# Kernel tuning notes

Hardware: AMD Instinct MI355X
Metric: run time of the kernel (lower is better)

The kernel has to match this reference:

```python
import jax, jax.numpy as jnp
import numpy as np

N = 50000      # nodes
E = 800000     # random edges (self-loops appended -> E + N total)
IN = 128       # in_channels
H = 1          # heads
C = 128        # out_channels per head
NEG_SLOPE = 0.2


def setup_inputs() -> dict:
    key = jax.random.key(0)
    k1, k2, k3, k4, k5 = jax.random.split(key, 5)
    x = jax.random.normal(k1, (N, IN), jnp.float32)
    src = jax.random.randint(k2, (E,), 0, N)
    dst = jax.random.randint(k3, (E,), 0, N)
    loops = jnp.arange(N)
    # PyG 1.3.2 GATConv adds self-loops before propagate
    edge_index = jnp.stack([jnp.concatenate([src, loops]),
                            jnp.concatenate([dst, loops])]).astype(jnp.int64)
    W = jax.random.normal(k4, (IN, H * C), jnp.float32) * np.float32(1.0 / np.sqrt(IN))
    att = jax.random.normal(k5, (H, 2 * C), jnp.float32) * np.float32(0.1)
    bias = jnp.zeros((H * C,), jnp.float32)
    return {"x": x, "edge_index": edge_index, "W": W, "att": att, "bias": bias}


def reference(x, edge_index, W, att, bias):
    h = (x @ W).reshape(-1, H, C)            # [N,H,C] transformed features
    src, dst = edge_index[0], edge_index[1]  # j -> i
    hi = h[dst]                              # [Etot,H,C] x_i gather
    hj = h[src]                              # [Etot,H,C] x_j gather
    # alpha = sum(cat(x_i,x_j) * att, -1)
    alpha = (jnp.einsum('ehc,hc->eh', hi, att[:, :C])
             + jnp.einsum('ehc,hc->eh', hj, att[:, C:]))
    alpha = jax.nn.leaky_relu(alpha, NEG_SLOPE)
    # segment softmax over destination node (stable)
    m = jax.ops.segment_max(alpha, dst, num_segments=N)
    m = jnp.where(jnp.isfinite(m), m, 0.0)   # guard empty segments
    a = jnp.exp(alpha - m[dst])
    s = jax.ops.segment_sum(a, dst, num_segments=N)
    a = a / (s[dst] + 1e-16)
    # weighted scatter-add aggregation
    out = jax.ops.segment_sum(hj * a[:, :, None], dst, num_segments=N)  # [N,H,C]
    return out.reshape(-1, H * C) + bias
```

## Files before the change

kernel.cpp:

```cpp
#include <hip/hip_runtime.h>
#include <math.h>


constexpr int CH = 128;
constexpr int BNODES = 64;
constexpr int CAP = 2048;
constexpr int SCAP = 3072;
constexpr int NBMAX = 1024;
constexpr int SCHUNK = 4096;
constexpr int WTS = 136;
constexpr unsigned SENT = 0xFFFFFFFFu;

typedef __attribute__((ext_vector_type(8))) short bf16x8;
typedef __attribute__((ext_vector_type(4))) float f32x4;

static __device__ __forceinline__ unsigned short f2bf(float f) {
    unsigned u = __float_as_uint(f);
    unsigned r = (u + 0x7fffu + ((u >> 16) & 1u)) >> 16;
    return (unsigned short)r;
}

__global__ __launch_bounds__(256) void wtzero_kernel(const float* __restrict__ W,
                                                     unsigned short* __restrict__ WT,
                                                     int* __restrict__ gcur, int nb) {
    const int T = blockIdx.x * 256 + threadIdx.x;
    if (T < nb) gcur[T] = 0;
    const int k = T >> 4;
    const int n8 = (T & 15) * 8;
    const float4 a = *(const float4*)&W[k * CH + n8];
    const float4 b = *(const float4*)&W[k * CH + n8 + 4];
    WT[(n8 + 0) * WTS + k] = f2bf(a.x);
    WT[(n8 + 1) * WTS + k] = f2bf(a.y);
    WT[(n8 + 2) * WTS + k] = f2bf(a.z);
    WT[(n8 + 3) * WTS + k] = f2bf(a.w);
    WT[(n8 + 4) * WTS + k] = f2bf(b.x);
    WT[(n8 + 5) * WTS + k] = f2bf(b.y);
    WT[(n8 + 6) * WTS + k] = f2bf(b.z);
    WT[(n8 + 7) * WTS + k] = f2bf(b.w);
}

__global__ __launch_bounds__(256) void gemm_scatter_kernel(const float* __restrict__ x,
                                                           const unsigned short* __restrict__ WT,
                                                           const float* __restrict__ att,
                                                           unsigned short* __restrict__ hb,
                                                           float* __restrict__ ad,
                                                           float* __restrict__ as_,
                                                           const int* __restrict__ src,
                                                           const int* __restrict__ dst,
                                                           int* __restrict__ gcur,
                                                           unsigned* __restrict__ recs,
                                                           int n, int etot, int nb, int sb) {
    __shared__ alignas(16) unsigned char smem[52224];
    const int tid = threadIdx.x;

    if ((int)blockIdx.x >= sb) {
        unsigned short* Wl = (unsigned short*)smem;
        unsigned short* Xs = (unsigned short*)(smem + 34816);
        {
            const uint4* s = (const uint4*)WT;
            uint4* d = (uint4*)Wl;
            for (int i = tid; i < CH * WTS / 8; i += 256) d[i] = s[i];
        }

        const int lane = tid & 63, wave = tid >> 6;
        const int m = lane & 15, quad = lane >> 4;
        const int tbase = ((int)blockIdx.x - sb) * 128;
        const int srow = tid >> 2, sseg = tid & 3;

        #pragma unroll 1
        for (int half = 0; half < 2; ++half) {
            __syncthreads();
            {
                const int grow = min(tbase + half * 64 + srow, n - 1);
                const float* gx = x + (size_t)grow * CH;
                unsigned short* xd = &Xs[srow * WTS];
                #pragma unroll
                for (int i = 0; i < 8; ++i) {
                    const int c = sseg * 4 + i * 16;
                    const float4 u = *(const float4*)&gx[c];
                    ushort4 hs;
                    hs.x = f2bf(u.x); hs.y = f2bf(u.y); hs.z = f2bf(u.z); hs.w = f2bf(u.w);
                    *(ushort4*)&xd[c] = hs;
                }
            }
            __syncthreads();

            const int row0 = tbase + half * 64 + wave * 16;
            f32x4 acc[8] = {};
            #pragma unroll
            for (int t = 0; t < 4; ++t) {
                const int kb = t * 32 + quad * 8;
                const bf16x8 afr = *(const bf16x8*)&Xs[(wave * 16 + m) * WTS + kb];
                #pragma unroll
                for (int nt = 0; nt < 8; ++nt) {
                    const bf16x8 bfr = *(const bf16x8*)&Wl[(nt * 16 + m) * WTS + kb];
                    acc[nt] = __builtin_amdgcn_mfma_f32_16x16x32_bf16(afr, bfr, acc[nt], 0, 0, 0);
                }
            }

            const int rbase = row0 + quad * 4;
            float pd[4] = {}, ps[4] = {};
            #pragma unroll
            for (int nt = 0; nt < 8; ++nt) {
                const int col = nt * 16 + m;
                const float atd = att[col], ats = att[CH + col];
                #pragma unroll
                for (int r = 0; r < 4; ++r) {
                    pd[r] = fmaf(acc[nt][r], atd, pd[r]);
                    ps[r] = fmaf(acc[nt][r], ats, ps[r]);
                    const int rr = rbase + r;
                    if (rr < n) hb[(size_t)rr * CH + col] = f2bf(acc[nt][r]);
                }
            }
            #pragma unroll
            for (int r = 0; r < 4; ++r) {
                #pragma unroll
                for (int off = 8; off >= 1; off >>= 1) {
                    pd[r] += __shfl_xor(pd[r], off, 64);
                    ps[r] += __shfl_xor(ps[r], off, 64);
                }
                const int rr = rbase + r;
                if (m == 0 && rr < n) { ad[rr] = pd[r]; as_[rr] = ps[r]; }
            }
        }
    } else {
        int* hist = (int*)smem;
        int* cur = hist + NBMAX;
        unsigned* rbuf = (unsigned*)(cur + NBMAX);
        const int e0 = (int)blockIdx.x * SCHUNK;
        for (int t = tid; t < nb; t += 256) hist[t] = 0;
        __syncthreads();
        for (int i = tid; i < SCHUNK; i += 256) {
            const int e = e0 + i;
            if (e < etot) {
                const int d = dst[e];
                rbuf[i] = ((unsigned)d << 16) | (unsigned)src[e];
                atomicAdd(&hist[d >> 6], 1);
            }
        }
        __syncthreads();
        for (int t = tid; t < nb; t += 256) {
            const int h = hist[t];
            cur[t] = h ? atomicAdd(&gcur[t], h) : 0;
        }
        __syncthreads();
        for (int i = tid; i < SCHUNK; i += 256) {
            const int e = e0 + i;
            if (e < etot) {
                const unsigned r = rbuf[i];
                const int d = (int)(r >> 16);
                const int b = d >> 6;
                const int pos = atomicAdd(&cur[b], 1);
                if (pos < CAP)
                    recs[(size_t)b * CAP + pos] = ((unsigned)(d & 63) << 16) | (r & 0xffffu);
            }
        }
    }
}

__global__ __launch_bounds__(512) void aggregate_kernel(const unsigned char* __restrict__ hwb,
                                                        const float* __restrict__ ad,
                                                        const float* __restrict__ as_,
                                                        const int* __restrict__ gcur,
                                                        const unsigned* __restrict__ recs,
                                                        const float* __restrict__ bias,
                                                        float* __restrict__ out, int n) {
    __shared__ alignas(16) unsigned sorted[SCAP];
    __shared__ alignas(16) float alphas[SCAP];
    __shared__ float adl[BNODES];
    __shared__ int cnt[BNODES], ofs[BNODES], cur[BNODES];
    __shared__ int nEp_s;
    const int b = blockIdx.x;
    const int tid = threadIdx.x, lane = tid & 63, wid = tid >> 6;
    const unsigned* br = recs + (size_t)b * CAP;
    int nE = gcur[b]; if (nE > CAP) nE = CAP;
    unsigned* stash = (unsigned*)alphas;

    if (tid < BNODES) {
        cnt[tid] = 0;
        const int node = b * BNODES + tid;
        adl[tid] = (node < n) ? ad[node] : 0.f;
    }
    __syncthreads();
    for (int i = tid; i < nE; i += 512) {
        const unsigned r = br[i];
        stash[i] = r;
        atomicAdd(&cnt[r >> 16], 1);
    }
    __syncthreads();
    if (wid == 0) {
        const int c = cnt[lane];
        const int cr = (c + 15) & ~15;
        int v = cr;
        #pragma unroll
        for (int off = 1; off < 64; off <<= 1) {
            const int u = __shfl_up(v, (unsigned)off, 64);
            if (lane >= off) v += u;
        }
        ofs[lane] = v - cr;
        cur[lane] = v - cr;
        if (lane == 63) nEp_s = v;
    }
    __syncthreads();
    const int nEp = nEp_s;
    for (int i = tid; i < nEp; i += 512) sorted[i] = SENT;
    __syncthreads();
    for (int i = tid; i < nE; i += 512) {
        const unsigned r = stash[i];
        const int pos = atomicAdd(&cur[r >> 16], 1);
        sorted[pos] = r;
    }
    __syncthreads();
    for (int i = tid; i < nEp; i += 512) {
        const unsigned r = sorted[i];
        float p = 0.f;
        unsigned so = 0u;
        if (r != SENT) {
            float a = adl[r >> 16] + as_[r & 0xffffu];
            a = (a >= 0.f) ? a : 0.2f * a;
            p = __expf(a);
            so = (r & 0xffffu) << 8;
        }
        alphas[i] = p;
        sorted[i] = so;
    }
    __syncthreads();

    const unsigned lane4 = (unsigned)lane * 4u;
    for (int ln = wid; ln < BNODES; ln += 8) {
        const int node = b * BNODES + ln;
        if (node >= n) break;
        const int start = ofs[ln];
        const int endp = start + ((cnt[ln] + 15) & ~15);

        float ssum = 0.f, acc0 = 0.f, acc1 = 0.f;
        for (int e = start; e < endp; e += 16) {
            const uint4 s0 = *(const uint4*)&sorted[e];
            const uint4 s1 = *(const uint4*)&sorted[e + 4];
            const uint4 s2 = *(const uint4*)&sorted[e + 8];
            const uint4 s3 = *(const uint4*)&sorted[e + 12];
            const float4 p0 = *(const float4*)&alphas[e];
            const float4 p1 = *(const float4*)&alphas[e + 4];
            const float4 p2 = *(const float4*)&alphas[e + 8];
            const float4 p3 = *(const float4*)&alphas[e + 12];
            unsigned g[16];
            g[0]  = *(const unsigned*)(hwb + (s0.x + lane4));
            g[1]  = *(const unsigned*)(hwb + (s0.y + lane4));
            g[2]  = *(const unsigned*)(hwb + (s0.z + lane4));
            g[3]  = *(const unsigned*)(hwb + (s0.w + lane4));
            g[4]  = *(const unsigned*)(hwb + (s1.x + lane4));
            g[5]  = *(const unsigned*)(hwb + (s1.y + lane4));
            g[6]  = *(const unsigned*)(hwb + (s1.z + lane4));
            g[7]  = *(const unsigned*)(hwb + (s1.w + lane4));
            g[8]  = *(const unsigned*)(hwb + (s2.x + lane4));
            g[9]  = *(const unsigned*)(hwb + (s2.y + lane4));
            g[10] = *(const unsigned*)(hwb + (s2.z + lane4));
            g[11] = *(const unsigned*)(hwb + (s2.w + lane4));
            g[12] = *(const unsigned*)(hwb + (s3.x + lane4));
            g[13] = *(const unsigned*)(hwb + (s3.y + lane4));
            g[14] = *(const unsigned*)(hwb + (s3.z + lane4));
            g[15] = *(const unsigned*)(hwb + (s3.w + lane4));
            ssum += (p0.x + p0.y + p0.z + p0.w) + (p1.x + p1.y + p1.z + p1.w)
                  + (p2.x + p2.y + p2.z + p2.w) + (p3.x + p3.y + p3.z + p3.w);
            const float p[16] = {p0.x, p0.y, p0.z, p0.w, p1.x, p1.y, p1.z, p1.w,
                                 p2.x, p2.y, p2.z, p2.w, p3.x, p3.y, p3.z, p3.w};
            #pragma unroll
            for (int j = 0; j < 16; ++j) {
                acc0 = fmaf(p[j], __uint_as_float((g[j] & 0xffffu) << 16), acc0);
                acc1 = fmaf(p[j], __uint_as_float(g[j] & 0xffff0000u), acc1);
            }
        }
        const float inv = 1.f / (ssum + 1e-16f);
        const float2 bv = *(const float2*)&bias[lane * 2];
        float2 o;
        o.x = fmaf(acc0, inv, bv.x);
        o.y = fmaf(acc1, inv, bv.y);
        *(float2*)&out[node * CH + lane * 2] = o;
    }
}

extern "C" void kernel_launch(void* const* d_in, const int* in_sizes, int n_in,
                              void* d_out, int out_size, void* d_ws, size_t ws_size,
                              hipStream_t stream) {
    const float* x    = (const float*)d_in[0];
    const int*   ei   = (const int*)d_in[1];
    const float* W    = (const float*)d_in[2];
    const float* att  = (const float*)d_in[3];
    const float* bias = (const float*)d_in[4];
    float* out = (float*)d_out;

    const int N_   = in_sizes[0] / CH;
    const int Etot = in_sizes[1] / 2;
    const int* src = ei;
    const int* dst = ei + Etot;
    const int nb = (N_ + BNODES - 1) / BNODES;
    const int gb = (N_ + 127) / 128;
    const int sb = (Etot + SCHUNK - 1) / SCHUNK;

    char* ws = (char*)d_ws;
    size_t off = 0;
    auto alloc = [&](size_t bytes) -> void* {
        void* p = ws + off;
        off = (off + bytes + 255) & ~(size_t)255;
        return p;
    };
    unsigned short* hb = (unsigned short*)alloc((size_t)N_ * CH * sizeof(unsigned short));
    unsigned short* WT = (unsigned short*)alloc((size_t)CH * WTS * sizeof(unsigned short));
    float* ad      = (float*)alloc((size_t)N_ * sizeof(float));
    float* as_     = (float*)alloc((size_t)N_ * sizeof(float));
    int*   gcur    = (int*)  alloc((size_t)nb * sizeof(int));
    unsigned* recs = (unsigned*)alloc((size_t)nb * CAP * sizeof(unsigned));
    (void)ws_size; (void)n_in; (void)out_size;

    wtzero_kernel<<<8, 256, 0, stream>>>(W, WT, gcur, nb);
    gemm_scatter_kernel<<<sb + gb, 256, 0, stream>>>(x, WT, att, hb, ad, as_,
                                                     src, dst, gcur, recs, N_, Etot, nb, sb);
    aggregate_kernel<<<nb, 512, 0, stream>>>((const unsigned char*)hb, ad, as_, gcur, recs, bias, out, N_);
}
```

Before: 134.8 us.

## Split wavefront into half-waves gathering 8-byte rows, pad segments to 8

The aggregation loop now splits each 64-lane wavefront into two halves. Each half handles alternate edges, and every lane loads 8 bytes (four bf16 channels) instead of 4, so there are half as many gather instructions per edge pair. The partial sums are combined with a cross-half shuffle, and the lower 32 lanes write float4 outputs. Per-node segments are padded to 8 instead of 16, which wastes fewer gather slots on sentinel edges. The softmax denominator now comes from shared-memory atomics during the alpha pass, which adds LDS atomic contention in exchange for dropping the per-iteration sum.

```diff
diff --git a/kernel.cpp b/kernel.cpp
--- a/kernel.cpp
+++ b/kernel.cpp
@@ -168,6 +168,7 @@
     __shared__ alignas(16) unsigned sorted[SCAP];
     __shared__ alignas(16) float alphas[SCAP];
     __shared__ float adl[BNODES];
+    __shared__ float ssumL[BNODES];
     __shared__ int cnt[BNODES], ofs[BNODES], cur[BNODES];
     __shared__ int nEp_s;
     const int b = blockIdx.x;
@@ -178,6 +179,7 @@
 
     if (tid < BNODES) {
         cnt[tid] = 0;
+        ssumL[tid] = 0.f;
         const int node = b * BNODES + tid;
         adl[tid] = (node < n) ? ad[node] : 0.f;
     }
@@ -190,7 +192,7 @@
     __syncthreads();
     if (wid == 0) {
         const int c = cnt[lane];
-        const int cr = (c + 15) & ~15;
+        const int cr = (c + 7) & ~7;
         int v = cr;
         #pragma unroll
         for (int off = 1; off < 64; off <<= 1) {
@@ -220,21 +222,25 @@
             a = (a >= 0.f) ? a : 0.2f * a;
             p = __expf(a);
             so = (r & 0xffffu) << 8;
+            atomicAdd(&ssumL[r >> 16], p);
         }
         alphas[i] = p;
         sorted[i] = so;
     }
     __syncthreads();
 
-    const unsigned lane4 = (unsigned)lane * 4u;
+    const unsigned half = (unsigned)(lane >> 5);
+    const unsigned lo8 = (unsigned)(lane & 31) * 8u;
     for (int ln = wid; ln < BNODES; ln += 8) {
         const int node = b * BNODES + ln;
         if (node >= n) break;
         const int start = ofs[ln];
-        const int endp = start + ((cnt[ln] + 15) & ~15);
-
-        float ssum = 0.f, acc0 = 0.f, acc1 = 0.f;
-        for (int e = start; e < endp; e += 16) {
+        const int cnt8 = (cnt[ln] + 7) & ~7;
+        const int end16 = start + (cnt8 & ~15);
+
+        float a0 = 0.f, a1 = 0.f, a2 = 0.f, a3 = 0.f;
+        int e = start;
+        for (; e < end16; e += 16) {
             const uint4 s0 = *(const uint4*)&sorted[e];
             const uint4 s1 = *(const uint4*)&sorted[e + 4];
             const uint4 s2 = *(const uint4*)&sorted[e + 8];
@@ -243,39 +249,111 @@
             const float4 p1 = *(const float4*)&alphas[e + 4];
             const float4 p2 = *(const float4*)&alphas[e + 8];
             const float4 p3 = *(const float4*)&alphas[e + 12];
-            unsigned g[16];
-            g[0]  = *(const unsigned*)(hwb + (s0.x + lane4));
-            g[1]  = *(const unsigned*)(hwb + (s0.y + lane4));
-            g[2]  = *(const unsigned*)(hwb + (s0.z + lane4));
-            g[3]  = *(const unsigned*)(hwb + (s0.w + lane4));
-            g[4]  = *(const unsigned*)(hwb + (s1.x + lane4));
-            g[5]  = *(const unsigned*)(hwb + (s1.y + lane4));
-            g[6]  = *(const unsigned*)(hwb + (s1.z + lane4));
-            g[7]  = *(const unsigned*)(hwb + (s1.w + lane4));
-            g[8]  = *(const unsigned*)(hwb + (s2.x + lane4));
-            g[9]  = *(const unsigned*)(hwb + (s2.y + lane4));
-            g[10] = *(const unsigned*)(hwb + (s2.z + lane4));
-            g[11] = *(const unsigned*)(hwb + (s2.w + lane4));
-            g[12] = *(const unsigned*)(hwb + (s3.x + lane4));
-            g[13] = *(const unsigned*)(hwb + (s3.y + lane4));
-            g[14] = *(const unsigned*)(hwb + (s3.z + lane4));
-            g[15] = *(const unsigned*)(hwb + (s3.w + lane4));
-            ssum += (p0.x + p0.y + p0.z + p0.w) + (p1.x + p1.y + p1.z + p1.w)
-                  + (p2.x + p2.y + p2.z + p2.w) + (p3.x + p3.y + p3.z + p3.w);
-            const float p[16] = {p0.x, p0.y, p0.z, p0.w, p1.x, p1.y, p1.z, p1.w,
-                                 p2.x, p2.y, p2.z, p2.w, p3.x, p3.y, p3.z, p3.w};
-            #pragma unroll
-            for (int j = 0; j < 16; ++j) {
-                acc0 = fmaf(p[j], __uint_as_float((g[j] & 0xffffu) << 16), acc0);
-                acc1 = fmaf(p[j], __uint_as_float(g[j] & 0xffff0000u), acc1);
-            }
-        }
-        const float inv = 1.f / (ssum + 1e-16f);
-        const float2 bv = *(const float2*)&bias[lane * 2];
-        float2 o;
-        o.x = fmaf(acc0, inv, bv.x);
-        o.y = fmaf(acc1, inv, bv.y);
-        *(float2*)&out[node * CH + lane * 2] = o;
+            const unsigned A0 = half ? s0.y : s0.x;
+            const unsigned A1 = half ? s0.w : s0.z;
+            const unsigned A2 = half ? s1.y : s1.x;
+            const unsigned A3 = half ? s1.w : s1.z;
+            const unsigned A4 = half ? s2.y : s2.x;
+            const unsigned A5 = half ? s2.w : s2.z;
+            const unsigned A6 = half ? s3.y : s3.x;
+            const unsigned A7 = half ? s3.w : s3.z;
+            const float q0 = half ? p0.y : p0.x;
+            const float q1 = half ? p0.w : p0.z;
+            const float q2 = half ? p1.y : p1.x;
+            const float q3 = half ? p1.w : p1.z;
+            const float q4 = half ? p2.y : p2.x;
+            const float q5 = half ? p2.w : p2.z;
+            const float q6 = half ? p3.y : p3.x;
+            const float q7 = half ? p3.w : p3.z;
+            const uint2 g0 = *(const uint2*)(hwb + A0 + lo8);
+            const uint2 g1 = *(const uint2*)(hwb + A1 + lo8);
+            const uint2 g2 = *(const uint2*)(hwb + A2 + lo8);
+            const uint2 g3 = *(const uint2*)(hwb + A3 + lo8);
+            const uint2 g4 = *(const uint2*)(hwb + A4 + lo8);
+            const uint2 g5 = *(const uint2*)(hwb + A5 + lo8);
+            const uint2 g6 = *(const uint2*)(hwb + A6 + lo8);
+            const uint2 g7 = *(const uint2*)(hwb + A7 + lo8);
+            a0 = fmaf(q0, __uint_as_float(g0.x << 16), a0);
+            a1 = fmaf(q0, __uint_as_float(g0.x & 0xffff0000u), a1);
+            a2 = fmaf(q0, __uint_as_float(g0.y << 16), a2);
+            a3 = fmaf(q0, __uint_as_float(g0.y & 0xffff0000u), a3);
+            a0 = fmaf(q1, __uint_as_float(g1.x << 16), a0);
+            a1 = fmaf(q1, __uint_as_float(g1.x & 0xffff0000u), a1);
+            a2 = fmaf(q1, __uint_as_float(g1.y << 16), a2);
+            a3 = fmaf(q1, __uint_as_float(g1.y & 0xffff0000u), a3);
+            a0 = fmaf(q2, __uint_as_float(g2.x << 16), a0);
+            a1 = fmaf(q2, __uint_as_float(g2.x & 0xffff0000u), a1);
+            a2 = fmaf(q2, __uint_as_float(g2.y << 16), a2);
+            a3 = fmaf(q2, __uint_as_float(g2.y & 0xffff0000u), a3);
+            a0 = fmaf(q3, __uint_as_float(g3.x << 16), a0);
+            a1 = fmaf(q3, __uint_as_float(g3.x & 0xffff0000u), a1);
+            a2 = fmaf(q3, __uint_as_float(g3.y << 16), a2);
+            a3 = fmaf(q3, __uint_as_float(g3.y & 0xffff0000u), a3);
+            a0 = fmaf(q4, __uint_as_float(g4.x << 16), a0);
+            a1 = fmaf(q4, __uint_as_float(g4.x & 0xffff0000u), a1);
+            a2 = fmaf(q4, __uint_as_float(g4.y << 16), a2);
+            a3 = fmaf(q4, __uint_as_float(g4.y & 0xffff0000u), a3);
+            a0 = fmaf(q5, __uint_as_float(g5.x << 16), a0);
+            a1 = fmaf(q5, __uint_as_float(g5.x & 0xffff0000u), a1);
+            a2 = fmaf(q5, __uint_as_float(g5.y << 16), a2);
+            a3 = fmaf(q5, __uint_as_float(g5.y & 0xffff0000u), a3);
+            a0 = fmaf(q6, __uint_as_float(g6.x << 16), a0);
+            a1 = fmaf(q6, __uint_as_float(g6.x & 0xffff0000u), a1);
+            a2 = fmaf(q6, __uint_as_float(g6.y << 16), a2);
+            a3 = fmaf(q6, __uint_as_float(g6.y & 0xffff0000u), a3);
+            a0 = fmaf(q7, __uint_as_float(g7.x << 16), a0);
+            a1 = fmaf(q7, __uint_as_float(g7.x & 0xffff0000u), a1);
+            a2 = fmaf(q7, __uint_as_float(g7.y << 16), a2);
+            a3 = fmaf(q7, __uint_as_float(g7.y & 0xffff0000u), a3);
+        }
+        if (cnt8 & 8) {
+            const uint4 s0 = *(const uint4*)&sorted[e];
+            const uint4 s1 = *(const uint4*)&sorted[e + 4];
+            const float4 p0 = *(const float4*)&alphas[e];
+            const float4 p1 = *(const float4*)&alphas[e + 4];
+            const unsigned A0 = half ? s0.y : s0.x;
+            const unsigned A1 = half ? s0.w : s0.z;
+            const unsigned A2 = half ? s1.y : s1.x;
+            const unsigned A3 = half ? s1.w : s1.z;
+            const float q0 = half ? p0.y : p0.x;
+            const float q1 = half ? p0.w : p0.z;
+            const float q2 = half ? p1.y : p1.x;
+            const float q3 = half ? p1.w : p1.z;
+            const uint2 g0 = *(const uint2*)(hwb + A0 + lo8);
+            const uint2 g1 = *(const uint2*)(hwb + A1 + lo8);
+            const uint2 g2 = *(const uint2*)(hwb + A2 + lo8);
+            const uint2 g3 = *(const uint2*)(hwb + A3 + lo8);
+            a0 = fmaf(q0, __uint_as_float(g0.x << 16), a0);
+            a1 = fmaf(q0, __uint_as_float(g0.x & 0xffff0000u), a1);
+            a2 = fmaf(q0, __uint_as_float(g0.y << 16), a2);
+            a3 = fmaf(q0, __uint_as_float(g0.y & 0xffff0000u), a3);
+            a0 = fmaf(q1, __uint_as_float(g1.x << 16), a0);
+            a1 = fmaf(q1, __uint_as_float(g1.x & 0xffff0000u), a1);
+            a2 = fmaf(q1, __uint_as_float(g1.y << 16), a2);
+            a3 = fmaf(q1, __uint_as_float(g1.y & 0xffff0000u), a3);
+            a0 = fmaf(q2, __uint_as_float(g2.x << 16), a0);
+            a1 = fmaf(q2, __uint_as_float(g2.x & 0xffff0000u), a1);
+            a2 = fmaf(q2, __uint_as_float(g2.y << 16), a2);
+            a3 = fmaf(q2, __uint_as_float(g2.y & 0xffff0000u), a3);
+            a0 = fmaf(q3, __uint_as_float(g3.x << 16), a0);
+            a1 = fmaf(q3, __uint_as_float(g3.x & 0xffff0000u), a1);
+            a2 = fmaf(q3, __uint_as_float(g3.y << 16), a2);
+            a3 = fmaf(q3, __uint_as_float(g3.y & 0xffff0000u), a3);
+        }
+        a0 += __shfl_xor(a0, 32, 64);
+        a1 += __shfl_xor(a1, 32, 64);
+        a2 += __shfl_xor(a2, 32, 64);
+        a3 += __shfl_xor(a3, 32, 64);
+        if (lane < 32) {
+            const float inv = 1.f / (ssumL[ln] + 1e-16f);
+            const float4 bv = *(const float4*)&bias[lane * 4];
+            float4 o;
+            o.x = fmaf(a0, inv, bv.x);
+            o.y = fmaf(a1, inv, bv.y);
+            o.z = fmaf(a2, inv, bv.z);
+            o.w = fmaf(a3, inv, bv.w);
+            *(float4*)&out[node * CH + lane * 4] = o;
+        }
     }
 }
 
```

Result: slower. 140.9 us (+4.5%).

## Fuse three kernels into one cooperative persistent kernel with grid syncs

Applied to the files above, without the earlier changes.

Merges the weight-transpose, GEMM/scatter, and aggregation kernels into a single cooperative kernel that loops over work items and separates phases with grid.sync. The goal is to remove two kernel launch gaps and the tail effects between stages. In exchange, the grid is capped by occupancy (smem 52KB limits blocks per CU), aggregation now uses 256 threads instead of 512, and grid-wide barriers add their own cost. It falls back to the old three-kernel path if the cooperative launch fails.

```diff
diff --git a/kernel.cpp b/kernel.cpp
--- a/kernel.cpp
+++ b/kernel.cpp
@@ -1,5 +1,8 @@
 #include <hip/hip_runtime.h>
+#include <hip/hip_cooperative_groups.h>
 #include <math.h>
+
+namespace cg = cooperative_groups;
 
 
 constexpr int CH = 128;
@@ -18,6 +21,273 @@
     unsigned u = __float_as_uint(f);
     unsigned r = (u + 0x7fffu + ((u >> 16) & 1u)) >> 16;
     return (unsigned short)r;
+}
+
+__global__ __launch_bounds__(256) void fused_kernel(
+    const float* __restrict__ x, const float* __restrict__ W,
+    const float* __restrict__ att, const float* __restrict__ bias,
+    const int* __restrict__ src, const int* __restrict__ dst,
+    unsigned short* __restrict__ WT, unsigned short* __restrict__ hb,
+    float* __restrict__ ad, float* __restrict__ as_,
+    int* __restrict__ gcur, unsigned* __restrict__ recs,
+    float* __restrict__ out,
+    int n, int etot, int nb, int sb, int gb)
+{
+    __shared__ alignas(16) unsigned char smem[52224];
+    const int tid = threadIdx.x;
+    cg::grid_group grid = cg::this_grid();
+
+    {
+        const int T = (int)blockIdx.x * 256 + tid;
+        if (T < 2048) {
+            if (T < nb) gcur[T] = 0;
+            const int k = T >> 4;
+            const int n8 = (T & 15) * 8;
+            const float4 a = *(const float4*)&W[k * CH + n8];
+            const float4 bq = *(const float4*)&W[k * CH + n8 + 4];
+            WT[(n8 + 0) * WTS + k] = f2bf(a.x);
+            WT[(n8 + 1) * WTS + k] = f2bf(a.y);
+            WT[(n8 + 2) * WTS + k] = f2bf(a.z);
+            WT[(n8 + 3) * WTS + k] = f2bf(a.w);
+            WT[(n8 + 4) * WTS + k] = f2bf(bq.x);
+            WT[(n8 + 5) * WTS + k] = f2bf(bq.y);
+            WT[(n8 + 6) * WTS + k] = f2bf(bq.z);
+            WT[(n8 + 7) * WTS + k] = f2bf(bq.w);
+        }
+    }
+    __threadfence();
+    grid.sync();
+    __threadfence();
+
+    for (int item = (int)blockIdx.x; item < sb + gb; item += (int)gridDim.x) {
+        __syncthreads();
+        if (item >= sb) {
+            unsigned short* Wl = (unsigned short*)smem;
+            unsigned short* Xs = (unsigned short*)(smem + 34816);
+            {
+                const uint4* s = (const uint4*)WT;
+                uint4* d = (uint4*)Wl;
+                for (int i = tid; i < CH * WTS / 8; i += 256) d[i] = s[i];
+            }
+            const int lane = tid & 63, wave = tid >> 6;
+            const int m = lane & 15, quad = lane >> 4;
+            const int tbase = (item - sb) * 128;
+            const int srow = tid >> 2, sseg = tid & 3;
+
+            #pragma unroll 1
+            for (int half = 0; half < 2; ++half) {
+                __syncthreads();
+                {
+                    const int grow = min(tbase + half * 64 + srow, n - 1);
+                    const float* gx = x + (size_t)grow * CH;
+                    unsigned short* xd = &Xs[srow * WTS];
+                    #pragma unroll
+                    for (int i = 0; i < 8; ++i) {
+                        const int c = sseg * 4 + i * 16;
+                        const float4 u = *(const float4*)&gx[c];
+                        ushort4 hs;
+                        hs.x = f2bf(u.x); hs.y = f2bf(u.y); hs.z = f2bf(u.z); hs.w = f2bf(u.w);
+                        *(ushort4*)&xd[c] = hs;
+                    }
+                }
+                __syncthreads();
+
+                const int row0 = tbase + half * 64 + wave * 16;
+                f32x4 acc[8] = {};
+                #pragma unroll
+                for (int t = 0; t < 4; ++t) {
+                    const int kb = t * 32 + quad * 8;
+                    const bf16x8 afr = *(const bf16x8*)&Xs[(wave * 16 + m) * WTS + kb];
+                    #pragma unroll
+                    for (int nt = 0; nt < 8; ++nt) {
+                        const bf16x8 bfr = *(const bf16x8*)&Wl[(nt * 16 + m) * WTS + kb];
+                        acc[nt] = __builtin_amdgcn_mfma_f32_16x16x32_bf16(afr, bfr, acc[nt], 0, 0, 0);
+                    }
+                }
+
+                const int rbase = row0 + quad * 4;
+                float pd[4] = {}, ps[4] = {};
+                #pragma unroll
+                for (int nt = 0; nt < 8; ++nt) {
+                    const int col = nt * 16 + m;
+                    const float atd = att[col], ats = att[CH + col];
+                    #pragma unroll
+                    for (int r = 0; r < 4; ++r) {
+                        pd[r] = fmaf(acc[nt][r], atd, pd[r]);
+                        ps[r] = fmaf(acc[nt][r], ats, ps[r]);
+                        const int rr = rbase + r;
+                        if (rr < n) hb[(size_t)rr * CH + col] = f2bf(acc[nt][r]);
+                    }
+                }
+                #pragma unroll
+                for (int r = 0; r < 4; ++r) {
+                    #pragma unroll
+                    for (int off = 8; off >= 1; off >>= 1) {
+                        pd[r] += __shfl_xor(pd[r], off, 64);
+                        ps[r] += __shfl_xor(ps[r], off, 64);
+                    }
+                    const int rr = rbase + r;
+                    if (m == 0 && rr < n) { ad[rr] = pd[r]; as_[rr] = ps[r]; }
+                }
+            }
+        } else {
+            int* hist = (int*)smem;
+            int* curh = hist + NBMAX;
+            unsigned* rbuf = (unsigned*)(curh + NBMAX);
+            const int e0 = item * SCHUNK;
+            for (int t = tid; t < nb; t += 256) hist[t] = 0;
+            __syncthreads();
+            for (int i = tid; i < SCHUNK; i += 256) {
+                const int e = e0 + i;
+                if (e < etot) {
+                    const int d = dst[e];
+                    rbuf[i] = ((unsigned)d << 16) | (unsigned)src[e];
+                    atomicAdd(&hist[d >> 6], 1);
+                }
+            }
+            __syncthreads();
+            for (int t = tid; t < nb; t += 256) {
+                const int h = hist[t];
+                curh[t] = h ? atomicAdd(&gcur[t], h) : 0;
+            }
+            __syncthreads();
+            for (int i = tid; i < SCHUNK; i += 256) {
+                const int e = e0 + i;
+                if (e < etot) {
+                    const unsigned r = rbuf[i];
+                    const int d = (int)(r >> 16);
+                    const int bk = d >> 6;
+                    const int pos = atomicAdd(&curh[bk], 1);
+                    if (pos < CAP)
+                        recs[(size_t)bk * CAP + pos] = ((unsigned)(d & 63) << 16) | (r & 0xffffu);
+                }
+            }
+        }
+    }
+    __threadfence();
+    grid.sync();
+    __threadfence();
+
+    {
+        const unsigned char* hwb = (const unsigned char*)hb;
+        unsigned* sorted = (unsigned*)smem;
+        float* alphas    = (float*)(smem + 12288);
+        float* adl       = (float*)(smem + 24576);
+        int* cnt         = (int*)(smem + 24832);
+        int* ofs         = (int*)(smem + 25088);
+        int* curq        = (int*)(smem + 25344);
+        int* nEp_s       = (int*)(smem + 25600);
+        const int lane = tid & 63, wid = tid >> 6;
+        const unsigned lane4 = (unsigned)lane * 4u;
+
+        for (int b = (int)blockIdx.x; b < nb; b += (int)gridDim.x) {
+            __syncthreads();
+            const unsigned* br = recs + (size_t)b * CAP;
+            int nE = gcur[b]; if (nE > CAP) nE = CAP;
+            unsigned* stash = (unsigned*)alphas;
+
+            if (tid < BNODES) {
+                cnt[tid] = 0;
+                const int node = b * BNODES + tid;
+                adl[tid] = (node < n) ? ad[node] : 0.f;
+            }
+            __syncthreads();
+            for (int i = tid; i < nE; i += 256) {
+                const unsigned r = br[i];
+                stash[i] = r;
+                atomicAdd(&cnt[r >> 16], 1);
+            }
+            __syncthreads();
+            if (wid == 0) {
+                const int c = cnt[lane];
+                const int cr = (c + 15) & ~15;
+                int v = cr;
+                #pragma unroll
+                for (int off = 1; off < 64; off <<= 1) {
+                    const int u = __shfl_up(v, (unsigned)off, 64);
+                    if (lane >= off) v += u;
+                }
+                ofs[lane] = v - cr;
+                curq[lane] = v - cr;
+                if (lane == 63) *nEp_s = v;
+            }
+            __syncthreads();
+            const int nEp = *nEp_s;
+            for (int i = tid; i < nEp; i += 256) sorted[i] = SENT;
+            __syncthreads();
+            for (int i = tid; i < nE; i += 256) {
+                const unsigned r = stash[i];
+                const int pos = atomicAdd(&curq[r >> 16], 1);
+                sorted[pos] = r;
+            }
+            __syncthreads();
+            for (int i = tid; i < nEp; i += 256) {
+                const unsigned r = sorted[i];
+                float p = 0.f;
+                unsigned so = 0u;
+                if (r != SENT) {
+                    float a = adl[r >> 16] + as_[r & 0xffffu];
+                    a = (a >= 0.f) ? a : 0.2f * a;
+                    p = __expf(a);
+                    so = (r & 0xffffu) << 8;
+                }
+                alphas[i] = p;
+                sorted[i] = so;
+            }
+            __syncthreads();
+
+            for (int ln = wid; ln < BNODES; ln += 4) {
+                const int node = b * BNODES + ln;
+                if (node >= n) break;
+                const int start = ofs[ln];
+                const int endp = start + ((cnt[ln] + 15) & ~15);
+
+                float ssum = 0.f, acc0 = 0.f, acc1 = 0.f;
+                for (int e = start; e < endp; e += 16) {
+                    const uint4 s0 = *(const uint4*)&sorted[e];
+                    const uint4 s1 = *(const uint4*)&sorted[e + 4];
+                    const uint4 s2 = *(const uint4*)&sorted[e + 8];
+                    const uint4 s3 = *(const uint4*)&sorted[e + 12];
+                    const float4 p0 = *(const float4*)&alphas[e];
+                    const float4 p1 = *(const float4*)&alphas[e + 4];
+                    const float4 p2 = *(const float4*)&alphas[e + 8];
+                    const float4 p3 = *(const float4*)&alphas[e + 12];
+                    unsigned g[16];
+                    g[0]  = *(const unsigned*)(hwb + (s0.x + lane4));
+                    g[1]  = *(const unsigned*)(hwb + (s0.y + lane4));
+                    g[2]  = *(const unsigned*)(hwb + (s0.z + lane4));
+                    g[3]  = *(const unsigned*)(hwb + (s0.w + lane4));
+                    g[4]  = *(const unsigned*)(hwb + (s1.x + lane4));
+                    g[5]  = *(const unsigned*)(hwb + (s1.y + lane4));
+                    g[6]  = *(const unsigned*)(hwb + (s1.z + lane4));
+                    g[7]  = *(const unsigned*)(hwb + (s1.w + lane4));
+                    g[8]  = *(const unsigned*)(hwb + (s2.x + lane4));
+                    g[9]  = *(const unsigned*)(hwb + (s2.y + lane4));
+                    g[10] = *(const unsigned*)(hwb + (s2.z + lane4));
+                    g[11] = *(const unsigned*)(hwb + (s2.w + lane4));
+                    g[12] = *(const unsigned*)(hwb + (s3.x + lane4));
+                    g[13] = *(const unsigned*)(hwb + (s3.y + lane4));
+                    g[14] = *(const unsigned*)(hwb + (s3.z + lane4));
+                    g[15] = *(const unsigned*)(hwb + (s3.w + lane4));
+                    ssum += (p0.x + p0.y + p0.z + p0.w) + (p1.x + p1.y + p1.z + p1.w)
+                          + (p2.x + p2.y + p2.z + p2.w) + (p3.x + p3.y + p3.z + p3.w);
+                    const float p[16] = {p0.x, p0.y, p0.z, p0.w, p1.x, p1.y, p1.z, p1.w,
+                                         p2.x, p2.y, p2.z, p2.w, p3.x, p3.y, p3.z, p3.w};
+                    #pragma unroll
+                    for (int j = 0; j < 16; ++j) {
+                        acc0 = fmaf(p[j], __uint_as_float((g[j] & 0xffffu) << 16), acc0);
+                        acc1 = fmaf(p[j], __uint_as_float(g[j] & 0xffff0000u), acc1);
+                    }
+                }
+                const float inv = 1.f / (ssum + 1e-16f);
+                const float2 bv = *(const float2*)&bias[lane * 2];
+                float2 o;
+                o.x = fmaf(acc0, inv, bv.x);
+                o.y = fmaf(acc1, inv, bv.y);
+                *(float2*)&out[(size_t)node * CH + lane * 2] = o;
+            }
+        }
+    }
 }
 
 __global__ __launch_bounds__(256) void wtzero_kernel(const float* __restrict__ W,
@@ -61,7 +331,6 @@
             uint4* d = (uint4*)Wl;
             for (int i = tid; i < CH * WTS / 8; i += 256) d[i] = s[i];
         }
-
         const int lane = tid & 63, wave = tid >> 6;
         const int m = lane & 15, quad = lane >> 4;
         const int tbase = ((int)blockIdx.x - sb) * 128;
@@ -289,13 +558,13 @@
     const float* bias = (const float*)d_in[4];
     float* out = (float*)d_out;
 
-    const int N_   = in_sizes[0] / CH;
-    const int Etot = in_sizes[1] / 2;
+    int N_   = in_sizes[0] / CH;
+    int Etot = in_sizes[1] / 2;
     const int* src = ei;
     const int* dst = ei + Etot;
-    const int nb = (N_ + BNODES - 1) / BNODES;
-    const int gb = (N_ + 127) / 128;
-    const int sb = (Etot + SCHUNK - 1) / SCHUNK;
+    int nb = (N_ + BNODES - 1) / BNODES;
+    int gb = (N_ + 127) / 128;
+    int sb = (Etot + SCHUNK - 1) / SCHUNK;
 
     char* ws = (char*)d_ws;
     size_t off = 0;
@@ -312,8 +581,49 @@
     unsigned* recs = (unsigned*)alloc((size_t)nb * CAP * sizeof(unsigned));
     (void)ws_size; (void)n_in; (void)out_size;
 
-    wtzero_kernel<<<8, 256, 0, stream>>>(W, WT, gcur, nb);
-    gemm_scatter_kernel<<<sb + gb, 256, 0, stream>>>(x, WT, att, hb, ad, as_,
-                                                     src, dst, gcur, recs, N_, Etot, nb, sb);
-    aggregate_kernel<<<nb, 512, 0, stream>>>((const unsigned char*)hb, ad, as_, gcur, recs, bias, out, N_);
+    static int coopBlocks = -1;
+    if (coopBlocks == -1) {
+        int bpc = 0;
+        if (hipOccupancyMaxActiveBlocksPerMultiprocessor(&bpc, fused_kernel, 256, 0) == hipSuccess
+            && bpc > 0) {
+            int dev = 0;
+            hipGetDevice(&dev);
+            hipDeviceProp_t prop;
+            int ncu = 256;
+            if (hipGetDeviceProperties(&prop, dev) == hipSuccess && prop.multiProcessorCount > 0)
+                ncu = prop.multiProcessorCount;
+            coopBlocks = bpc * ncu;
+        } else {
+            coopBlocks = 0;
+        }
+    }
+
+    bool launched = false;
+    if (coopBlocks > 0) {
+        int need = sb + gb;
+        if (nb > need) need = nb;
+        if (need < 8) need = 8;
+        int grid = coopBlocks < need ? coopBlocks : need;
+        void* args[] = {
+            (void*)&x, (void*)&W, (void*)&att, (void*)&bias,
+            (void*)&src, (void*)&dst,
+            (void*)&WT, (void*)&hb, (void*)&ad, (void*)&as_,
+            (void*)&gcur, (void*)&recs, (void*)&out,
+            (void*)&N_, (void*)&Etot, (void*)&nb, (void*)&sb, (void*)&gb
+        };
+        if (hipLaunchCooperativeKernel(fused_kernel, dim3(grid), dim3(256),
+                                       args, 0, stream) == hipSuccess) {
+            launched = true;
+        } else {
+            coopBlocks = 0;
+        }
+    }
+
+    if (!launched) {
+        wtzero_kernel<<<8, 256, 0, stream>>>(W, WT, gcur, nb);
+        gemm_scatter_kernel<<<sb + gb, 256, 0, stream>>>(x, WT, att, hb, ad, as_,
+                                                         src, dst, gcur, recs, N_, Etot, nb, sb);
+        aggregate_kernel<<<nb, 512, 0, stream>>>((const unsigned char*)hb, ad, as_,
+                                                 gcur, recs, bias, out, N_);
+    }
 }
```

Result: slower. 328.7 us (+143.8%).
